# Kernel optimization log

Hardware: AMD Instinct MI355X
Metric: run time of the kernel (lower is better)

Reference implementation:

```python
import jax, jax.numpy as jnp
import numpy as np

EPS = 1e-6
D = 100   # embed_dim
P = 10    # perspective


def _cos(v1, v2):
    # cosine over last dim with broadcasting; clamp sum-of-squares at EPS (as torch)
    num = (v1 * v2).sum(-1)
    n1 = jnp.sqrt(jnp.clip((v1 * v1).sum(-1), EPS, None))
    n2 = jnp.sqrt(jnp.clip((v2 * v2).sum(-1), EPS, None))
    return num / (n1 * n2)


def _cosine_matrix(s1, s2):
    # [n1,B,D] x [n2,B,D] -> [n1,n2,B]; einsum avoids the [n1,n2,B,D] intermediate
    num = jnp.einsum('ibd,jbd->ijb', s1, s2)
    n1 = jnp.sqrt(jnp.clip((s1 * s1).sum(-1), EPS, None))  # [n1,B]
    n2 = jnp.sqrt(jnp.clip((s2 * s2).sum(-1), EPS, None))  # [n2,B]
    return num / (n1[:, None] * n2[None])


def _full(s1, s2, w):
    ws1 = s1[:, :, None, :] * w            # [n1,B,P,D]
    ws2 = s2[-1][:, None, :] * w           # [B,P,D]
    return _cos(ws1, ws2[None])            # [n1,B,P]


def _maxpool(s1, s2, w):
    # cos[i,j,b,p] between s1[i,b]*w[p] and s2[j,b]*w[p], without the 5-D intermediate
    w2 = w * w
    num = jnp.einsum('ibd,jbd,pd->ijbp', s1, s2, w2)
    n1 = jnp.sqrt(jnp.clip(jnp.einsum('ibd,pd->ibp', s1 * s1, w2), EPS, None))
    n2 = jnp.sqrt(jnp.clip(jnp.einsum('jbd,pd->jbp', s2 * s2, w2), EPS, None))
    cos = num / (n1[:, None] * n2[None])
    return cos.max(1)                      # [n1,B,P]


def _mean_att(s1, s2, w, cosm):
    # attentive vector: cosine-weighted mean of s2 states -> [n1,B,D]
    att = jnp.einsum('ijb,jbd->ibd', cosm, s2) / (cosm.sum(1) + EPS)[..., None]
    return _cos(s1[:, :, None, :] * w, att[:, :, None, :] * w)


def _max_att(s1, s2, w, cosm):
    n1, B = cosm.shape[0], s2.shape[1]
    idx = jnp.argmax(cosm, axis=1).reshape(-1)  # values in [0, n_state2)
    # NOTE: faithful to the torch source, which indexes the flattened [n2*B, D]
    # view of s2 with per-state indices (a bug in the original, reproduced here).
    att = s2.reshape(-1, D)[idx].reshape(n1, B, D)
    return _cos(s1[:, :, None, :] * w, att[:, :, None, :] * w)


def setup_inputs() -> dict:
    key = jax.random.key(0)
    ks = jax.random.split(key, 10)
    s1 = jax.random.normal(ks[0], (100, 256, 2 * D), dtype=jnp.float32)
    s2 = jax.random.normal(ks[1], (100, 256, 2 * D), dtype=jnp.float32)
    ws = {f'w{i+1}': jax.random.uniform(ks[2 + i], (P, D), dtype=jnp.float32,
                                        minval=-0.01, maxval=0.01) for i in range(8)}
    return {'s1': s1, 's2': s2, **ws}


def reference(s1, s2, w1, w2, w3, w4, w5, w6, w7, w8):
    s1f, s1b = s1[..., :D], s1[..., D:]
    s2f, s2b = s2[..., :D], s2[..., D:]
    cosf = _cosine_matrix(s1f, s2f)
    cosb = _cosine_matrix(s1b, s2b)
    full = jnp.concatenate([_full(s1f, s2f, w1), _full(s1b, s2b, w2)], 2)
    maxp = jnp.concatenate([_maxpool(s1f, s2f, w3), _maxpool(s1b, s2b, w4)], 2)
    mean_a = jnp.concatenate([_mean_att(s1f, s2f, w5, cosf), _mean_att(s1b, s2b, w6, cosb)], 2)
    # original forward uses mean_attentive for the backward half of max-attentive (bug kept)
    max_a = jnp.concatenate([_max_att(s1f, s2f, w7, cosf), _mean_att(s1b, s2b, w8, cosb)], 2)
    # `type` in the original forward shadows the builtin, so the 'all' branch always runs
    return jnp.concatenate([full, maxp, mean_a, max_a], axis=-1)  # [n1,B,8P]
```

## Files before the change

### kernel.cpp

```cpp
#include <hip/hip_runtime.h>

#define TT 100
#define DD 100
#define DC 25
#define PP 10
#define BBATCH 256
#define OC 80
#define NW 8

typedef float v2f __attribute__((ext_vector_type(2)));
typedef float v4f __attribute__((ext_vector_type(4)));

static constexpr float FEPS = 1e-6f;

__device__ __forceinline__ int   f2i(float x) { return __builtin_bit_cast(int, x); }
__device__ __forceinline__ float i2f(int x)   { return __builtin_bit_cast(float, x); }

#define ROR_F(v, ctrl) i2f(__builtin_amdgcn_update_dpp(0, f2i(v), (ctrl), 0xf, 0xf, false))
#define ROR_I(v, ctrl) __builtin_amdgcn_update_dpp(0, (v), (ctrl), 0xf, 0xf, false)

__device__ __forceinline__ v2f xswap32_f(float v) {
#if __has_builtin(__builtin_amdgcn_permlane32_swap)
  auto pr = __builtin_amdgcn_permlane32_swap((unsigned)f2i(v), (unsigned)f2i(v), false, false);
  v2f r; r.x = i2f((int)pr[0]); r.y = i2f((int)pr[1]);
  return r;
#else
  v2f r; r.x = v; r.y = __shfl_xor(v, 32, 64);
  return r;
#endif
}

__device__ __forceinline__ float wave_sum(float v) {
  v += ROR_F(v, 0x121);
  v += ROR_F(v, 0x122);
  v += ROR_F(v, 0x124);
  v += ROR_F(v, 0x128);
  v += i2f(__builtin_amdgcn_ds_swizzle(f2i(v), 0x401f));
  v2f s = xswap32_f(v);
  return s.x + s.y;
}

__device__ __forceinline__ float wave_max(float v) {
  v = fmaxf(v, ROR_F(v, 0x121));
  v = fmaxf(v, ROR_F(v, 0x122));
  v = fmaxf(v, ROR_F(v, 0x124));
  v = fmaxf(v, ROR_F(v, 0x128));
  v = fmaxf(v, i2f(__builtin_amdgcn_ds_swizzle(f2i(v), 0x401f)));
  v2f s = xswap32_f(v);
  return fmaxf(s.x, s.y);
}

__device__ __forceinline__ void amax2(float& v, int& i, float ov, int oi) {
  if (ov > v || (ov == v && oi < i)) { v = ov; i = oi; }
}

__device__ __forceinline__ void wave_argmax(float& v, int& idx) {
  amax2(v, idx, ROR_F(v, 0x121), ROR_I(idx, 0x121));
  amax2(v, idx, ROR_F(v, 0x122), ROR_I(idx, 0x122));
  amax2(v, idx, ROR_F(v, 0x124), ROR_I(idx, 0x124));
  amax2(v, idx, ROR_F(v, 0x128), ROR_I(idx, 0x128));
  amax2(v, idx, i2f(__builtin_amdgcn_ds_swizzle(f2i(v), 0x401f)),
        __builtin_amdgcn_ds_swizzle(idx, 0x401f));
#if __has_builtin(__builtin_amdgcn_permlane32_swap)
  {
    auto rv = __builtin_amdgcn_permlane32_swap((unsigned)f2i(v), (unsigned)f2i(v), false, false);
    auto ri = __builtin_amdgcn_permlane32_swap((unsigned)idx, (unsigned)idx, false, false);
    amax2(v, idx, i2f((int)rv[0]), (int)ri[0]);
    amax2(v, idx, i2f((int)rv[1]), (int)ri[1]);
  }
#else
  amax2(v, idx, __shfl_xor(v, 32, 64), __shfl_xor(idx, 32, 64));
#endif
}

__global__ __launch_bounds__(512, 2) void match_kernel(
    const float* __restrict__ s1, const float* __restrict__ s2,
    const float* __restrict__ w1, const float* __restrict__ w2,
    const float* __restrict__ w3, const float* __restrict__ w4,
    const float* __restrict__ w5, const float* __restrict__ w6,
    const float* __restrict__ w7, const float* __restrict__ w8,
    float* __restrict__ out)
{
  const int dir  = blockIdx.x & 1;
  const int b    = blockIdx.x >> 1;
  const int doff = dir * DD;
  const int tid  = threadIdx.x;
  const int lane = tid & 63;
  const int wv   = tid >> 6;

  const float* wfull = dir ? w2 : w1;
  const float* wmax  = dir ? w4 : w3;
  const float* wmean = dir ? w6 : w5;
  const float* watt2 = dir ? w8 : w7;

  __shared__ __align__(16) float S2V[DC][TT + 1][4];
  __shared__ __align__(16) float W2SQ[PP][DD];
  __shared__ float N2PI[TT];
  __shared__ float N2WI[TT][11];
  __shared__ __align__(16) float S1R[4 * NW][DD];
  __shared__ __align__(16) float CROW[4 * NW][DD];
  __shared__ float N1PI[4 * NW];
  __shared__ float N1WI[4 * NW][PP];
  __shared__ int   ARGJ[4 * NW];

  for (int idx = tid; idx < TT * DD; idx += 512) {
    int j = idx / DD, d = idx - j * DD;
    S2V[d >> 2][j][d & 3] = s2[(j * BBATCH + b) * (2 * DD) + doff + d];
  }
  for (int idx = tid; idx < PP * DD; idx += 512) {
    int p = idx / DD, d = idx - p * DD;
    float v = wmax[idx];
    W2SQ[p][d] = v * v;
  }
  __syncthreads();

  for (int task = tid; task < TT + TT * PP; task += 512) {
    if (task < TT) {
      int j = task;
      float a = 0.f;
      for (int c = 0; c < DC; ++c) {
        v4f f = *(const v4f*)&S2V[c][j][0];
#pragma unroll
        for (int k = 0; k < 4; ++k) a = fmaf(f[k], f[k], a);
      }
      N2PI[j] = 1.0f / sqrtf(fmaxf(a, FEPS));
    } else {
      int q = task - TT; int j = q / PP, p = q - j * PP;
      float a = 0.f;
      for (int c = 0; c < DC; ++c) {
        v4f f = *(const v4f*)&S2V[c][j][0];
        v4f w = *(const v4f*)&W2SQ[p][4 * c];
#pragma unroll
        for (int k = 0; k < 4; ++k) a = fmaf(f[k] * f[k], w[k], a);
      }
      N2WI[j][p] = rsqrtf(fmaxf(a, FEPS));
    }
  }
  __syncthreads();

  const int  j0   = lane;
  const int  j1   = 64 + lane;
  const bool act1 = (j1 < TT);
  const int  j1c  = act1 ? j1 : (TT - 1);
  const bool actd = (64 + lane) < DD;
  const int  d1   = actd ? (64 + lane) : (DD - 1);
  const int  c0i  = lane >> 2, k0 = lane & 3;
  const int  c1i  = d1 >> 2,   k1 = d1 & 3;

  const int sl = wv * 4;

  for (int g = wv; g < 25; g += NW) {
    const int i0 = g * 4;

    for (int q = lane; q < 4 * DC; q += 64) {
      int rr = q / DC, c = q - rr * DC;
      *(v4f*)&S1R[sl + rr][4 * c] =
          *(const v4f*)&s1[((i0 + rr) * BBATCH + b) * (2 * DD) + doff + 4 * c];
    }

    if (lane < 4 * 11) {
      int rr = lane / 11, q = lane - rr * 11;
      if (q == 0) {
        float a = 0.f;
        for (int c = 0; c < DC; ++c) {
          v4f f = *(const v4f*)&S1R[sl + rr][4 * c];
#pragma unroll
          for (int k = 0; k < 4; ++k) a = fmaf(f[k], f[k], a);
        }
        N1PI[sl + rr] = 1.0f / sqrtf(fmaxf(a, FEPS));
      } else {
        int p = q - 1;
        float a = 0.f;
        for (int c = 0; c < DC; ++c) {
          v4f f = *(const v4f*)&S1R[sl + rr][4 * c];
          v4f w = *(const v4f*)&W2SQ[p][4 * c];
#pragma unroll
          for (int k = 0; k < 4; ++k) a = fmaf(f[k] * f[k], w[k], a);
        }
        N1WI[sl + rr][p] = rsqrtf(fmaxf(a, FEPS));
      }
    }

    float rs[4] = {0, 0, 0, 0};
    v2f attp[4] = {{0, 0}, {0, 0}, {0, 0}, {0, 0}};

    v2f dotp[4] = {{0, 0}, {0, 0}, {0, 0}, {0, 0}};
    v2f wap[4][PP];
#pragma unroll
    for (int r = 0; r < 4; ++r)
#pragma unroll
      for (int p = 0; p < PP; ++p) wap[r][p] = (v2f){0.f, 0.f};

    for (int c = 0; c < DC; ++c) {
      v4f s2a4 = *(const v4f*)&S2V[c][j0][0];
      v4f s2b4 = *(const v4f*)&S2V[c][j1c][0];
      v4f wq[PP];
#pragma unroll
      for (int p = 0; p < PP; ++p) wq[p] = *(const v4f*)&W2SQ[p][4 * c];
      v4f s1v[4];
#pragma unroll
      for (int r = 0; r < 4; ++r) s1v[r] = *(const v4f*)&S1R[sl + r][4 * c];
#pragma unroll
      for (int k = 0; k < 4; ++k) {
        v2f s2ab; s2ab.x = s2a4[k]; s2ab.y = s2b4[k];
#pragma unroll
        for (int r = 0; r < 4; ++r) {
          v2f s1xx; s1xx.x = s1v[r][k]; s1xx.y = s1v[r][k];
          v2f ta = s1xx * s2ab;
          dotp[r] += ta;
#pragma unroll
          for (int p = 0; p < PP; ++p) {
            v2f wk; wk.x = wq[p][k]; wk.y = wq[p][k];
            wap[r][p] = __builtin_elementwise_fma(ta, wk, wap[r][p]);
          }
        }
      }
    }

#pragma unroll
    for (int r = 0; r < 4; ++r) {
      float n1pi_r = N1PI[sl + r];
      float c0 = dotp[r].x * (n1pi_r * N2PI[j0]);
      float c1 = dotp[r].y * (n1pi_r * N2PI[j1c]);
      CROW[sl + r][j0] = c0;
      if (act1) CROW[sl + r][j1] = c1;
      rs[r] = wave_sum(c0 + (act1 ? c1 : 0.f));

      float mv = c0; int mi = j0;
      if (act1 && (c1 > mv)) { mv = c1; mi = j1; }
      wave_argmax(mv, mi);
      if (lane == 0) ARGJ[sl + r] = mi;

#pragma unroll
      for (int p = 0; p < PP; ++p) {
        float v0 = wap[r][p].x * N2WI[j0][p];
        float v1 = act1 ? wap[r][p].y * N2WI[j1c][p] : -3.4e38f;
        float m = wave_max(fmaxf(v0, v1));
        if (lane == 0) {
          out[((i0 + r) * BBATCH + b) * OC + 20 + dir * PP + p] = m * N1WI[sl + r][p];
        }
      }
    }

    for (int j = 0; j < TT; ++j) {
      v2f s2ab; s2ab.x = S2V[c0i][j][k0]; s2ab.y = S2V[c1i][j][k1];
#pragma unroll
      for (int r = 0; r < 4; ++r) {
        float cv = CROW[sl + r][j];
        v2f cc; cc.x = cv; cc.y = cv;
        attp[r] = __builtin_elementwise_fma(cc, s2ab, attp[r]);
      }
    }

#pragma unroll
    for (int r = 0; r < 4; ++r) {
      float inv = 1.0f / (rs[r] + FEPS);
      CROW[sl + r][lane] = attp[r].x * inv;
      if (actd) CROW[sl + r][64 + lane] = attp[r].y * inv;
    }

    for (int tk = lane; tk < 120; tk += 64) {
      int r = tk / 30;
      int q = tk - r * 30;
      int set = q / PP;
      int p = q - set * PP;
      const float* wrow = (set == 0 ? wfull : (set == 1 ? wmean : watt2)) + p * DD;
      const float* gat = s2 + ARGJ[sl + r] * (2 * DD);
      float num = 0.f, nx = 0.f, ny = 0.f;
      for (int c = 0; c < DC; ++c) {
        v4f x4 = *(const v4f*)&S1R[sl + r][4 * c];
        v4f y4;
        if (set == 0)                     y4 = *(const v4f*)&S2V[c][TT - 1][0];
        else if (set == 1 || dir == 1)    y4 = *(const v4f*)&CROW[sl + r][4 * c];
        else                              y4 = *(const v4f*)&gat[4 * c];
        v4f w4 = *(const v4f*)&wrow[4 * c];
#pragma unroll
        for (int k = 0; k < 4; ++k) {
          float w2v = w4[k] * w4[k];
          num = fmaf(x4[k] * y4[k], w2v, num);
          nx  = fmaf(x4[k] * x4[k], w2v, nx);
          ny  = fmaf(y4[k] * y4[k], w2v, ny);
        }
      }
      float cres = num * rsqrtf(fmaxf(nx, FEPS)) * rsqrtf(fmaxf(ny, FEPS));
      int ch = (set == 0 ? 0 : (set == 1 ? 40 : 60)) + dir * PP + p;
      out[((i0 + r) * BBATCH + b) * OC + ch] = cres;
    }
  }
}

extern "C" void kernel_launch(void* const* d_in, const int* in_sizes, int n_in,
                              void* d_out, int out_size, void* d_ws, size_t ws_size,
                              hipStream_t stream) {
  const float* s1 = (const float*)d_in[0];
  const float* s2 = (const float*)d_in[1];
  match_kernel<<<dim3(512), dim3(512), 0, stream>>>(
      s1, s2,
      (const float*)d_in[2], (const float*)d_in[3],
      (const float*)d_in[4], (const float*)d_in[5],
      (const float*)d_in[6], (const float*)d_in[7],
      (const float*)d_in[8], (const float*)d_in[9],
      (float*)d_out);
}
```

Before: 416.8 us.

## Rebalance row work across waves and vectorize perspective accumulators via transposed weights

Redistributes the 100 s1 rows among the 8 waves so that each wave processes 12 or 13 rows, in chunks of 4 plus a single-row tail. Previously it was 25 groups of 4 rows round-robin, so one wave got 4 groups while the others got 3. Adds a transposed squared-weight table so the perspective weights load as packed vectors, and pairs perspectives rather than j values in the packed FMAs. The body becomes a templated lambda instantiated for 4 rows and 1 row, which increases code size and may raise register pressure.

```diff
diff --git a/kernel.cpp b/kernel.cpp
--- a/kernel.cpp
+++ b/kernel.cpp
@@ -12,6 +12,8 @@
 typedef float v4f __attribute__((ext_vector_type(4)));
 
 static constexpr float FEPS = 1e-6f;
+
+template<int N> struct IC { static constexpr int v = N; };
 
 __device__ __forceinline__ int   f2i(float x) { return __builtin_bit_cast(int, x); }
 __device__ __forceinline__ float i2f(int x)   { return __builtin_bit_cast(float, x); }
@@ -95,6 +97,7 @@
 
   __shared__ __align__(16) float S2V[DC][TT + 1][4];
   __shared__ __align__(16) float W2SQ[PP][DD];
+  __shared__ __align__(16) float W2T[DC][4][PP];
   __shared__ float N2PI[TT];
   __shared__ float N2WI[TT][11];
   __shared__ __align__(16) float S1R[4 * NW][DD];
@@ -110,7 +113,9 @@
   for (int idx = tid; idx < PP * DD; idx += 512) {
     int p = idx / DD, d = idx - p * DD;
     float v = wmax[idx];
-    W2SQ[p][d] = v * v;
+    float v2 = v * v;
+    W2SQ[p][d] = v2;
+    W2T[d >> 2][d & 3][p] = v2;
   }
   __syncthreads();
 
@@ -149,16 +154,16 @@
 
   const int sl = wv * 4;
 
-  for (int g = wv; g < 25; g += NW) {
-    const int i0 = g * 4;
-
-    for (int q = lane; q < 4 * DC; q += 64) {
+  auto body = [&](auto ic, const int i0) {
+    constexpr int NR = decltype(ic)::v;
+
+    for (int q = lane; q < NR * DC; q += 64) {
       int rr = q / DC, c = q - rr * DC;
       *(v4f*)&S1R[sl + rr][4 * c] =
           *(const v4f*)&s1[((i0 + rr) * BBATCH + b) * (2 * DD) + doff + 4 * c];
     }
 
-    if (lane < 4 * 11) {
+    if (lane < NR * 11) {
       int rr = lane / 11, q = lane - rr * 11;
       if (q == 0) {
         float a = 0.f;
@@ -181,47 +186,58 @@
       }
     }
 
-    float rs[4] = {0, 0, 0, 0};
-    v2f attp[4] = {{0, 0}, {0, 0}, {0, 0}, {0, 0}};
-
-    v2f dotp[4] = {{0, 0}, {0, 0}, {0, 0}, {0, 0}};
-    v2f wap[4][PP];
-#pragma unroll
-    for (int r = 0; r < 4; ++r)
-#pragma unroll
-      for (int p = 0; p < PP; ++p) wap[r][p] = (v2f){0.f, 0.f};
+    float dot0[NR], dot1[NR];
+    v2f wap[NR][2][5];
+#pragma unroll
+    for (int r = 0; r < NR; ++r) {
+      dot0[r] = 0.f; dot1[r] = 0.f;
+#pragma unroll
+      for (int pp = 0; pp < 5; ++pp) {
+        wap[r][0][pp] = (v2f){0.f, 0.f};
+        wap[r][1][pp] = (v2f){0.f, 0.f};
+      }
+    }
 
     for (int c = 0; c < DC; ++c) {
       v4f s2a4 = *(const v4f*)&S2V[c][j0][0];
       v4f s2b4 = *(const v4f*)&S2V[c][j1c][0];
-      v4f wq[PP];
-#pragma unroll
-      for (int p = 0; p < PP; ++p) wq[p] = *(const v4f*)&W2SQ[p][4 * c];
-      v4f s1v[4];
-#pragma unroll
-      for (int r = 0; r < 4; ++r) s1v[r] = *(const v4f*)&S1R[sl + r][4 * c];
+      v4f s1v[NR];
+#pragma unroll
+      for (int r = 0; r < NR; ++r) s1v[r] = *(const v4f*)&S1R[sl + r][4 * c];
 #pragma unroll
       for (int k = 0; k < 4; ++k) {
-        v2f s2ab; s2ab.x = s2a4[k]; s2ab.y = s2b4[k];
-#pragma unroll
-        for (int r = 0; r < 4; ++r) {
-          v2f s1xx; s1xx.x = s1v[r][k]; s1xx.y = s1v[r][k];
-          v2f ta = s1xx * s2ab;
-          dotp[r] += ta;
-#pragma unroll
-          for (int p = 0; p < PP; ++p) {
-            v2f wk; wk.x = wq[p][k]; wk.y = wq[p][k];
-            wap[r][p] = __builtin_elementwise_fma(ta, wk, wap[r][p]);
+        v4f wA = *(const v4f*)&W2T[c][k][0];
+        v4f wB = *(const v4f*)&W2T[c][k][4];
+        v2f wC = *(const v2f*)&W2T[c][k][8];
+        v2f wp[5];
+        wp[0] = __builtin_shufflevector(wA, wA, 0, 1);
+        wp[1] = __builtin_shufflevector(wA, wA, 2, 3);
+        wp[2] = __builtin_shufflevector(wB, wB, 0, 1);
+        wp[3] = __builtin_shufflevector(wB, wB, 2, 3);
+        wp[4] = wC;
+#pragma unroll
+        for (int r = 0; r < NR; ++r) {
+          float ta0 = s1v[r][k] * s2a4[k];
+          float ta1 = s1v[r][k] * s2b4[k];
+          dot0[r] += ta0;
+          dot1[r] += ta1;
+          v2f t0; t0.x = ta0; t0.y = ta0;
+          v2f t1; t1.x = ta1; t1.y = ta1;
+#pragma unroll
+          for (int pp = 0; pp < 5; ++pp) {
+            wap[r][0][pp] = __builtin_elementwise_fma(t0, wp[pp], wap[r][0][pp]);
+            wap[r][1][pp] = __builtin_elementwise_fma(t1, wp[pp], wap[r][1][pp]);
           }
         }
       }
     }
 
-#pragma unroll
-    for (int r = 0; r < 4; ++r) {
+    float rs[NR];
+#pragma unroll
+    for (int r = 0; r < NR; ++r) {
       float n1pi_r = N1PI[sl + r];
-      float c0 = dotp[r].x * (n1pi_r * N2PI[j0]);
-      float c1 = dotp[r].y * (n1pi_r * N2PI[j1c]);
+      float c0 = dot0[r] * (n1pi_r * N2PI[j0]);
+      float c1 = dot1[r] * (n1pi_r * N2PI[j1c]);
       CROW[sl + r][j0] = c0;
       if (act1) CROW[sl + r][j1] = c1;
       rs[r] = wave_sum(c0 + (act1 ? c1 : 0.f));
@@ -233,8 +249,10 @@
 
 #pragma unroll
       for (int p = 0; p < PP; ++p) {
-        float v0 = wap[r][p].x * N2WI[j0][p];
-        float v1 = act1 ? wap[r][p].y * N2WI[j1c][p] : -3.4e38f;
+        float a0 = (p & 1) ? wap[r][0][p >> 1].y : wap[r][0][p >> 1].x;
+        float a1 = (p & 1) ? wap[r][1][p >> 1].y : wap[r][1][p >> 1].x;
+        float v0 = a0 * N2WI[j0][p];
+        float v1 = act1 ? a1 * N2WI[j1c][p] : -3.4e38f;
         float m = wave_max(fmaxf(v0, v1));
         if (lane == 0) {
           out[((i0 + r) * BBATCH + b) * OC + 20 + dir * PP + p] = m * N1WI[sl + r][p];
@@ -242,24 +260,28 @@
       }
     }
 
+    float att0[NR], att1[NR];
+#pragma unroll
+    for (int r = 0; r < NR; ++r) { att0[r] = 0.f; att1[r] = 0.f; }
     for (int j = 0; j < TT; ++j) {
-      v2f s2ab; s2ab.x = S2V[c0i][j][k0]; s2ab.y = S2V[c1i][j][k1];
-#pragma unroll
-      for (int r = 0; r < 4; ++r) {
+      float s2d0 = S2V[c0i][j][k0];
+      float s2d1 = S2V[c1i][j][k1];
+#pragma unroll
+      for (int r = 0; r < NR; ++r) {
         float cv = CROW[sl + r][j];
-        v2f cc; cc.x = cv; cc.y = cv;
-        attp[r] = __builtin_elementwise_fma(cc, s2ab, attp[r]);
-      }
-    }
-
-#pragma unroll
-    for (int r = 0; r < 4; ++r) {
+        att0[r] = fmaf(cv, s2d0, att0[r]);
+        att1[r] = fmaf(cv, s2d1, att1[r]);
+      }
+    }
+
+#pragma unroll
+    for (int r = 0; r < NR; ++r) {
       float inv = 1.0f / (rs[r] + FEPS);
-      CROW[sl + r][lane] = attp[r].x * inv;
-      if (actd) CROW[sl + r][64 + lane] = attp[r].y * inv;
-    }
-
-    for (int tk = lane; tk < 120; tk += 64) {
+      CROW[sl + r][lane] = att0[r] * inv;
+      if (actd) CROW[sl + r][64 + lane] = att1[r] * inv;
+    }
+
+    for (int tk = lane; tk < NR * 30; tk += 64) {
       int r = tk / 30;
       int q = tk - r * 30;
       int set = q / PP;
@@ -286,7 +308,11 @@
       int ch = (set == 0 ? 0 : (set == 1 ? 40 : 60)) + dir * PP + p;
       out[((i0 + r) * BBATCH + b) * OC + ch] = cres;
     }
-  }
+  };
+
+  const int start = wv * 12 + (wv > 4 ? wv - 4 : 0);
+  for (int it = 0; it < 3; ++it) body(IC<4>{}, start + it * 4);
+  if (wv >= 4) body(IC<1>{}, start + 12);
 }
 
 extern "C" void kernel_launch(void* const* d_in, const int* in_sizes, int n_in,
```

Measured after the change: 809.0 us. 94.1% more time.

## Rebalance row groups across waves with a templated remainder body

Applied to the files above, without the earlier changes.

Replaces the strided 4-row group loop, where wave 0 handled four groups and the others three, with contiguous per-wave ranges. Each wave now handles 12 rows, and waves 4-7 take one extra row. The body becomes a lambda templated on the row count, so the single-row tail is compiled separately. The attentive accumulation also switches from packed v2f FMAs to scalar FMAs. The aim is to shorten the slowest wave's critical path, at the cost of a less efficient single-row pass and more code size.

```diff
diff --git a/kernel.cpp b/kernel.cpp
--- a/kernel.cpp
+++ b/kernel.cpp
@@ -12,6 +12,8 @@
 typedef float v4f __attribute__((ext_vector_type(4)));
 
 static constexpr float FEPS = 1e-6f;
+
+template<int N> struct IC { static constexpr int v = N; };
 
 __device__ __forceinline__ int   f2i(float x) { return __builtin_bit_cast(int, x); }
 __device__ __forceinline__ float i2f(int x)   { return __builtin_bit_cast(float, x); }
@@ -149,16 +151,16 @@
 
   const int sl = wv * 4;
 
-  for (int g = wv; g < 25; g += NW) {
-    const int i0 = g * 4;
-
-    for (int q = lane; q < 4 * DC; q += 64) {
+  auto body = [&](auto ic, const int i0) {
+    constexpr int NR = decltype(ic)::v;
+
+    for (int q = lane; q < NR * DC; q += 64) {
       int rr = q / DC, c = q - rr * DC;
       *(v4f*)&S1R[sl + rr][4 * c] =
           *(const v4f*)&s1[((i0 + rr) * BBATCH + b) * (2 * DD) + doff + 4 * c];
     }
 
-    if (lane < 4 * 11) {
+    if (lane < NR * 11) {
       int rr = lane / 11, q = lane - rr * 11;
       if (q == 0) {
         float a = 0.f;
@@ -181,15 +183,14 @@
       }
     }
 
-    float rs[4] = {0, 0, 0, 0};
-    v2f attp[4] = {{0, 0}, {0, 0}, {0, 0}, {0, 0}};
-
-    v2f dotp[4] = {{0, 0}, {0, 0}, {0, 0}, {0, 0}};
-    v2f wap[4][PP];
-#pragma unroll
-    for (int r = 0; r < 4; ++r)
+    v2f dotp[NR];
+    v2f wap[NR][PP];
+#pragma unroll
+    for (int r = 0; r < NR; ++r) {
+      dotp[r] = (v2f){0.f, 0.f};
 #pragma unroll
       for (int p = 0; p < PP; ++p) wap[r][p] = (v2f){0.f, 0.f};
+    }
 
     for (int c = 0; c < DC; ++c) {
       v4f s2a4 = *(const v4f*)&S2V[c][j0][0];
@@ -197,14 +198,14 @@
       v4f wq[PP];
 #pragma unroll
       for (int p = 0; p < PP; ++p) wq[p] = *(const v4f*)&W2SQ[p][4 * c];
-      v4f s1v[4];
-#pragma unroll
-      for (int r = 0; r < 4; ++r) s1v[r] = *(const v4f*)&S1R[sl + r][4 * c];
+      v4f s1v[NR];
+#pragma unroll
+      for (int r = 0; r < NR; ++r) s1v[r] = *(const v4f*)&S1R[sl + r][4 * c];
 #pragma unroll
       for (int k = 0; k < 4; ++k) {
         v2f s2ab; s2ab.x = s2a4[k]; s2ab.y = s2b4[k];
 #pragma unroll
-        for (int r = 0; r < 4; ++r) {
+        for (int r = 0; r < NR; ++r) {
           v2f s1xx; s1xx.x = s1v[r][k]; s1xx.y = s1v[r][k];
           v2f ta = s1xx * s2ab;
           dotp[r] += ta;
@@ -217,8 +218,9 @@
       }
     }
 
-#pragma unroll
-    for (int r = 0; r < 4; ++r) {
+    float rs[NR];
+#pragma unroll
+    for (int r = 0; r < NR; ++r) {
       float n1pi_r = N1PI[sl + r];
       float c0 = dotp[r].x * (n1pi_r * N2PI[j0]);
       float c1 = dotp[r].y * (n1pi_r * N2PI[j1c]);
@@ -242,24 +244,28 @@
       }
     }
 
+    float att0[NR], att1[NR];
+#pragma unroll
+    for (int r = 0; r < NR; ++r) { att0[r] = 0.f; att1[r] = 0.f; }
     for (int j = 0; j < TT; ++j) {
-      v2f s2ab; s2ab.x = S2V[c0i][j][k0]; s2ab.y = S2V[c1i][j][k1];
-#pragma unroll
-      for (int r = 0; r < 4; ++r) {
+      float s2d0 = S2V[c0i][j][k0];
+      float s2d1 = S2V[c1i][j][k1];
+#pragma unroll
+      for (int r = 0; r < NR; ++r) {
         float cv = CROW[sl + r][j];
-        v2f cc; cc.x = cv; cc.y = cv;
-        attp[r] = __builtin_elementwise_fma(cc, s2ab, attp[r]);
-      }
-    }
-
-#pragma unroll
-    for (int r = 0; r < 4; ++r) {
+        att0[r] = fmaf(cv, s2d0, att0[r]);
+        att1[r] = fmaf(cv, s2d1, att1[r]);
+      }
+    }
+
+#pragma unroll
+    for (int r = 0; r < NR; ++r) {
       float inv = 1.0f / (rs[r] + FEPS);
-      CROW[sl + r][lane] = attp[r].x * inv;
-      if (actd) CROW[sl + r][64 + lane] = attp[r].y * inv;
-    }
-
-    for (int tk = lane; tk < 120; tk += 64) {
+      CROW[sl + r][lane] = att0[r] * inv;
+      if (actd) CROW[sl + r][64 + lane] = att1[r] * inv;
+    }
+
+    for (int tk = lane; tk < NR * 30; tk += 64) {
       int r = tk / 30;
       int q = tk - r * 30;
       int set = q / PP;
@@ -286,7 +292,11 @@
       int ch = (set == 0 ? 0 : (set == 1 ? 40 : 60)) + dir * PP + p;
       out[((i0 + r) * BBATCH + b) * OC + ch] = cres;
     }
-  }
+  };
+
+  const int start = wv * 12 + (wv > 4 ? wv - 4 : 0);
+  for (int it = 0; it < 3; ++it) body(IC<4>{}, start + it * 4);
+  if (wv >= 4) body(IC<1>{}, start + 12);
 }
 
 extern "C" void kernel_launch(void* const* d_in, const int* in_sizes, int n_in,
```

New measurement: 807.1 us. 93.7% more time.
